# Kernel optimization log

Hardware: AMD Instinct MI355X
Metric: run time of the kernel (lower is better)

## Reference

```python
import jax, jax.numpy as jnp
import numpy as np
import math

DIM = 384
NH = 6
DH = DIM // NH
B = 2
S = 2048
EPS = 1e-6
LN_EPS = 1e-5


def setup_inputs() -> dict:
    key = jax.random.key(0)
    ks = jax.random.split(key, 8)
    q = jax.random.normal(ks[0], (B, S, DIM), dtype=jnp.float32)
    k = jax.random.normal(ks[1], (B, S, DIM), dtype=jnp.float32)
    v = jax.random.normal(ks[2], (B, S, DIM), dtype=jnp.float32)
    # gate linear params (Linear(3*dim, num_heads)); small random weights to exercise the math
    igate_w = jax.random.normal(ks[3], (NH, 3 * DIM), dtype=jnp.float32) * 0.02
    igate_b = jax.random.normal(ks[4], (NH,), dtype=jnp.float32) * 0.1
    fgate_w = jax.random.normal(ks[5], (NH, 3 * DIM), dtype=jnp.float32) * 0.02
    fgate_b = jnp.linspace(3.0, 6.0, NH, dtype=jnp.float32)
    # MultiHeadLayerNorm residual weight (stored as delta, effective scale = 1 + w)
    outnorm_weight = jax.random.normal(ks[6], (DIM,), dtype=jnp.float32) * 0.02
    return {"q": q, "k": k, "v": v, "igate_w": igate_w, "igate_b": igate_b,
            "fgate_w": fgate_w, "fgate_b": fgate_b, "outnorm_weight": outnorm_weight}


def _mlstm_forward(q, k, v, igate_w, igate_b, fgate_w, fgate_b, outnorm_weight):
    Bq, Sq, _ = q.shape
    gate_in = jnp.concatenate([q, k, v], axis=-1)                       # (B,S,3D)
    ig = gate_in @ igate_w.T + igate_b                                   # (B,S,NH)
    fg = gate_in @ fgate_w.T + fgate_b                                   # (B,S,NH)
    # split heads: (B,NH,S,DH)
    qh = q.reshape(Bq, Sq, NH, DH).transpose(0, 2, 1, 3)
    kh = k.reshape(Bq, Sq, NH, DH).transpose(0, 2, 1, 3)
    vh = v.reshape(Bq, Sq, NH, DH).transpose(0, 2, 1, 3)
    ig = ig.transpose(0, 2, 1)                                           # (B,NH,S)
    fg = fg.transpose(0, 2, 1)                                           # (B,NH,S)

    log_fg = jax.nn.log_sigmoid(fg)                                      # (B,NH,S)
    lfc = jnp.concatenate([jnp.zeros((Bq, NH, 1), dtype=q.dtype),
                           jnp.cumsum(log_fg, axis=-1)], axis=-1)        # (B,NH,S+1)
    # log_fg_matrix[i,j] = cumsum[i] - cumsum[j] (sliced [1:,1:]), masked causal
    diff = lfc[:, :, 1:, None] - lfc[:, :, None, 1:]                     # (B,NH,S,S)
    ltr = jnp.tril(jnp.ones((Sq, Sq), dtype=bool))
    log_fg_mat = jnp.where(ltr, diff, -jnp.inf)
    log_D = log_fg_mat + ig[:, :, None, :]                               # + igate^T
    max_log_D = jnp.max(log_D, axis=-1, keepdims=True)                   # rowwise stabilize
    D = jnp.exp(log_D - max_log_D)
    qk = jnp.einsum('bhsd,bhtd->bhst', qh, kh) / math.sqrt(DH)
    C = qk * D
    normalizer = jnp.maximum(jnp.abs(jnp.sum(C, axis=-1, keepdims=True)),
                             jnp.exp(-max_log_D))
    h = jnp.einsum('bhst,bhtd->bhsd', C / (normalizer + EPS), vh)        # (B,NH,S,DH)

    # MultiHeadLayerNorm == group_norm over each head's DH channels, scale=(1+w)
    mean = jnp.mean(h, axis=-1, keepdims=True)
    var = jnp.var(h, axis=-1, keepdims=True)
    normed = (h - mean) / jnp.sqrt(var + LN_EPS)
    scale = (1.0 + outnorm_weight).reshape(NH, DH)[None, :, None, :]
    out = normed * scale
    return out.transpose(0, 2, 1, 3).reshape(Bq, Sq, DIM)


def reference(q, k, v, igate_w, igate_b, fgate_w, fgate_b, outnorm_weight):
    return _mlstm_forward(q, k, v, igate_w, igate_b, fgate_w, fgate_b, outnorm_weight)
```

## Files before the change

### kernel.cpp

```cpp
#include <hip/hip_runtime.h>
#include <math.h>

#define DIM 384
#define NH 6
#define DH 64
#define B_ 2
#define S_ 2048
#define EPS 1e-6f
#define LN_EPS 1e-5f
#define G3 (3*DIM)
#define LOG2E 1.44269504f
#define KSTR 72
#define NT (S_/64)
#define NSPLIT 4
#define NBH (B_*NH)

typedef __attribute__((ext_vector_type(8))) short bf16x8;
typedef __attribute__((ext_vector_type(4))) short bf16x4;
typedef __attribute__((ext_vector_type(4))) float f32x4;
typedef __attribute__((ext_vector_type(8))) unsigned short u16x8;

__device__ __forceinline__ unsigned short f2bf(float f){
    unsigned int u = __float_as_uint(f);
    u += 0x7fff + ((u >> 16) & 1);
    return (unsigned short)(u >> 16);
}
__device__ __forceinline__ float bf2f(unsigned short u){
    return __uint_as_float(((unsigned int)u) << 16);
}
__device__ __forceinline__ float logsig(float x){
    return fminf(x, 0.f) - log1pf(expf(-fabsf(x)));
}

__global__ __launch_bounds__(256) void vt_kernel(
    const float* __restrict__ v, unsigned short* __restrict__ Vt) {
    __shared__ unsigned short lt[64*KSTR];
    int bh = blockIdx.y;
    int b = bh / NH, h = bh % NH;
    int t0 = blockIdx.x * 64;
    int tid = threadIdx.x;
    #pragma unroll
    for (int i = 0; i < 4; i++){
        int idx = tid + 256*i;
        int r = idx >> 4;
        int c4 = (idx & 15) * 4;
        float4 x = *(const float4*)(v + ((size_t)b*S_ + t0 + r)*DIM + h*DH + c4);
        lt[(c4+0)*KSTR + r] = f2bf(x.x);
        lt[(c4+1)*KSTR + r] = f2bf(x.y);
        lt[(c4+2)*KSTR + r] = f2bf(x.z);
        lt[(c4+3)*KSTR + r] = f2bf(x.w);
    }
    __syncthreads();
    #pragma unroll
    for (int i = 0; i < 2; i++){
        int idx = tid + 256*i;
        int d = idx >> 3;
        int t8 = (idx & 7) * 8;
        u16x8 o = *(const u16x8*)&lt[d*KSTR + t8];
        *(u16x8*)(Vt + (size_t)bh*DH*S_ + (size_t)d*S_ + t0 + t8) = o;
    }
}

__global__ __launch_bounds__(256) void gates_kernel(
    const float* __restrict__ q, const float* __restrict__ k, const float* __restrict__ v,
    const float* __restrict__ iw, const float* __restrict__ ib,
    const float* __restrict__ fw, const float* __restrict__ fb,
    float* __restrict__ ig_out, float* __restrict__ lf_out,
    unsigned short* __restrict__ Qb, unsigned short* __restrict__ Kb) {
    int wave = (blockIdx.x * 256 + threadIdx.x) >> 6;
    int lane = threadIdx.x & 63;
    int b = wave / S_, s = wave % S_;
    size_t base = ((size_t)b * S_ + s) * DIM;
    float aI[NH], aF[NH];
    #pragma unroll
    for (int h = 0; h < NH; h++){ aI[h] = 0.f; aF[h] = 0.f; }
    for (int g = lane; g < G3/4; g += 64) {
        int e = g * 4;
        float4 x4;
        if (e < DIM){
            x4 = *(const float4*)(q + base + e);
            ushort4 t; t.x=f2bf(x4.x*0.125f); t.y=f2bf(x4.y*0.125f);
            t.z=f2bf(x4.z*0.125f); t.w=f2bf(x4.w*0.125f);
            *(ushort4*)(Qb + base + e) = t;
        } else if (e < 2*DIM){
            x4 = *(const float4*)(k + base + e - DIM);
            ushort4 t; t.x=f2bf(x4.x); t.y=f2bf(x4.y); t.z=f2bf(x4.z); t.w=f2bf(x4.w);
            *(ushort4*)(Kb + base + e - DIM) = t;
        } else {
            x4 = *(const float4*)(v + base + e - 2*DIM);
        }
        #pragma unroll
        for (int h = 0; h < NH; h++){
            float4 wi = *(const float4*)(iw + h*G3 + e);
            float4 wf = *(const float4*)(fw + h*G3 + e);
            aI[h] = fmaf(x4.x, wi.x, fmaf(x4.y, wi.y, fmaf(x4.z, wi.z, fmaf(x4.w, wi.w, aI[h]))));
            aF[h] = fmaf(x4.x, wf.x, fmaf(x4.y, wf.y, fmaf(x4.z, wf.z, fmaf(x4.w, wf.w, aF[h]))));
        }
    }
    #pragma unroll
    for (int h = 0; h < NH; h++){
        #pragma unroll
        for (int off = 32; off >= 1; off >>= 1){
            aI[h] += __shfl_xor(aI[h], off, 64);
            aF[h] += __shfl_xor(aF[h], off, 64);
        }
    }
    if (lane == 0) {
        #pragma unroll
        for (int h = 0; h < NH; h++){
            ig_out[((size_t)b*NH + h)*S_ + s] = aI[h] + ib[h];
            lf_out[((size_t)b*NH + h)*S_ + s] = logsig(aF[h] + fb[h]);
        }
    }
}

__global__ __launch_bounds__(256) void scan_kernel(
    const float* __restrict__ lf, const float* __restrict__ ig,
    float* __restrict__ cum, float* __restrict__ e2, float* __restrict__ pm,
    float* __restrict__ me, float* __restrict__ baseA){
    int bh = blockIdx.x;
    const float* srcL = lf + (size_t)bh * S_;
    const float* srcI = ig + (size_t)bh * S_;
    float* dstC = cum + (size_t)bh * S_;
    float* dstE = e2 + (size_t)bh * S_;
    float* dstP = pm + (size_t)bh * S_;
    int tid = threadIdx.x;
    float loc[8];
    float run = 0.f;
    #pragma unroll
    for (int j = 0; j < 8; j++){ run += srcL[tid*8 + j]; loc[j] = run; }
    __shared__ float sm[256];
    sm[tid] = run;
    __syncthreads();
    float total = run;
    for (int off = 1; off < 256; off <<= 1){
        float vv = (tid >= off) ? sm[tid - off] : 0.f;
        __syncthreads();
        sm[tid] += vv;
        __syncthreads();
    }
    float excl = sm[tid] - total;
    float c[8];
    #pragma unroll
    for (int j = 0; j < 8; j++){ c[j] = excl + loc[j]; dstC[tid*8 + j] = c[j]; }
    __shared__ float sb[32];
    if ((tid & 7) == 0) sb[tid >> 3] = excl;
    __syncthreads();
    float base_t = sb[tid >> 3];
    float E[8], mloc = -INFINITY;
    #pragma unroll
    for (int j = 0; j < 8; j++){
        E[j] = srcI[tid*8 + j] - c[j] + base_t;
        dstE[tid*8 + j] = exp2f(E[j] * LOG2E);
        mloc = fmaxf(mloc, E[j]);
    }
    __shared__ float smax[256];
    smax[tid] = mloc;
    __syncthreads();
    float carry = -INFINITY;
    int g0 = tid & ~7;
    for (int u = g0; u < tid; u++) carry = fmaxf(carry, smax[u]);
    float runm = carry;
    #pragma unroll
    for (int j = 0; j < 8; j++){
        runm = fmaxf(runm, E[j]);
        dstP[tid*8 + j] = runm;
    }
    if ((tid & 7) == 7) me[bh*NT + (tid >> 3)] = runm;
    if ((tid & 7) == 0) baseA[bh*NT + (tid >> 3)] = base_t;
}

__global__ __launch_bounds__(256) void mlstm_part(
    const unsigned short* __restrict__ Qb, const unsigned short* __restrict__ Kb,
    const unsigned short* __restrict__ Vt,
    const float* __restrict__ cum, const float* __restrict__ e2,
    const float* __restrict__ pm, const float* __restrict__ me,
    const float* __restrict__ baseA,
    unsigned short* __restrict__ pOb, float* __restrict__ pM, float* __restrict__ pL) {
    int lin = blockIdx.x;
    int sp  = lin / NBH;
    int bh  = lin % NBH;
    int st  = (NT - 1) - (sp >> 2);
    int c   = sp & 3;
    int L   = (st + 4) >> 2;
    int tb0 = c * L;
    int tb1 = min((c + 1) * L, st + 1);
    int pblk = lin;
    int tid = threadIdx.x;

    if (tb0 >= tb1){
        if (tid < 64){ pM[pblk*64 + tid] = -INFINITY; pL[pblk*64 + tid] = 0.f; }
        return;
    }

    __shared__ unsigned short kt[2][64*KSTR];
    __shared__ unsigned short vt[2][64*KSTR];

    int b = bh / NH, h = bh % NH;
    int s0 = st * 64;
    int wv   = tid >> 6;
    int lane = tid & 63;
    int lq   = lane & 15;
    int quad = lane >> 4;

    const unsigned short* kbT = Kb + (size_t)b*S_*DIM + h*DH;
    const unsigned short* vtB = Vt + (size_t)bh*DH*S_;
    const float* cmb = cum + (size_t)bh*S_;
    const float* e2b = e2 + (size_t)bh*S_;
    const float* meB = me + bh*NT;
    const float* baseB = baseA + bh*NT;

    int s_glob = s0 + 16*wv + lq;

    bf16x8 qf[2];
    {
        const unsigned short* qr = Qb + ((size_t)b*S_ + s_glob)*DIM + h*DH;
        qf[0] = *(const bf16x8*)(qr + 8*quad);
        qf[1] = *(const bf16x8*)(qr + 32 + 8*quad);
    }

    float cq   = cmb[s_glob];
    float pm_s = pm[(size_t)bh*S_ + s_glob];
    float m_s = -INFINITY, b_s = 0.f;
    f32x4 oacc[4];
    #pragma unroll
    for (int cg = 0; cg < 4; cg++) oacc[cg] = (f32x4){0.f,0.f,0.f,0.f};

    int sr[2], sc[2];
    #pragma unroll
    for (int i = 0; i < 2; i++){
        int idx = tid + 256*i;
        sr[i] = idx >> 3;
        sc[i] = (idx & 7) * 8;
    }

    u16x8 kreg[2], vreg[2];
    {
        const unsigned short* kb = kbT + (size_t)(tb0*64)*DIM;
        const unsigned short* vb = vtB + tb0*64;
        #pragma unroll
        for (int i = 0; i < 2; i++){
            kreg[i] = *(const u16x8*)(kb + (size_t)sr[i]*DIM + sc[i]);
            vreg[i] = *(const u16x8*)(vb + (size_t)sr[i]*S_ + sc[i]);
        }
        #pragma unroll
        for (int i = 0; i < 2; i++){
            *(u16x8*)&kt[0][sr[i]*KSTR + sc[i]] = kreg[i];
            *(u16x8*)&vt[0][sr[i]*KSTR + sc[i]] = vreg[i];
        }
    }
    __syncthreads();

    int bufi = 0;
    for (int t0 = tb0*64; t0 < tb1*64; t0 += 64){
        bool more = (t0 + 64 < tb1*64);
        if (more){
            const unsigned short* kb = kbT + (size_t)(t0 + 64)*DIM;
            const unsigned short* vb = vtB + (t0 + 64);
            #pragma unroll
            for (int i = 0; i < 2; i++){
                kreg[i] = *(const u16x8*)(kb + (size_t)sr[i]*DIM + sc[i]);
                vreg[i] = *(const u16x8*)(vb + (size_t)sr[i]*S_ + sc[i]);
            }
        }

        int tix = t0 >> 6;
        float base_t = baseB[tix];
        float me_t   = meB[tix];
        float4 e2v[4];
        #pragma unroll
        for (int tb = 0; tb < 4; tb++)
            e2v[tb] = *(const float4*)(e2b + t0 + 16*tb + 4*quad);

        const unsigned short* ktc = kt[bufi];
        const unsigned short* vtc = vt[bufi];
        f32x4 st4[4];
        #pragma unroll
        for (int tb = 0; tb < 4; tb++) st4[tb] = (f32x4){0.f,0.f,0.f,0.f};
        #pragma unroll
        for (int ks = 0; ks < 2; ks++){
            #pragma unroll
            for (int tb = 0; tb < 4; tb++){
                bf16x8 af = *(const bf16x8*)&ktc[(16*tb + lq)*KSTR + 32*ks + 8*quad];
                st4[tb] = __builtin_amdgcn_mfma_f32_16x16x32_bf16(af, qf[ks], st4[tb], 0, 0, 0);
            }
        }

        bool diag = (t0 == s0);
        float A = cq - base_t;
        float pmax = A + (diag ? pm_s : me_t);
        float mn = fmaxf(m_s, pmax);
        float sc2 = exp2f((m_s - mn) * LOG2E);
        float ws = exp2f((A - mn) * LOG2E);
        m_s = mn;
        float pv[4][4];
        #pragma unroll
        for (int tb = 0; tb < 4; tb++)
            #pragma unroll
            for (int r = 0; r < 4; r++)
                pv[tb][r] = st4[tb][r] * (ws * e2v[tb][r]);
        if (diag){
            #pragma unroll
            for (int tb = 0; tb < 4; tb++)
                #pragma unroll
                for (int r = 0; r < 4; r++)
                    if (t0 + 16*tb + 4*quad + r > s_glob) pv[tb][r] = 0.f;
        }
        float rs = 0.f;
        bf16x4 pf[4];
        #pragma unroll
        for (int tb = 0; tb < 4; tb++){
            #pragma unroll
            for (int r = 0; r < 4; r++){
                rs += pv[tb][r];
                pf[tb][r] = (short)f2bf(pv[tb][r]);
            }
        }
        rs += __shfl_xor(rs, 16, 64);
        rs += __shfl_xor(rs, 32, 64);
        b_s = b_s * sc2 + rs;

        #pragma unroll
        for (int r = 0; r < 4; r++){
            float sco = __shfl(sc2, 20*quad + r, 64);
            #pragma unroll
            for (int cg = 0; cg < 4; cg++) oacc[cg][r] *= sco;
        }

        #pragma unroll
        for (int tb = 0; tb < 4; tb++){
            #pragma unroll
            for (int cg = 0; cg < 4; cg++){
                bf16x4 vf = *(const bf16x4*)&vtc[(16*cg + lq)*KSTR + 16*tb + 4*quad];
                oacc[cg] = __builtin_amdgcn_mfma_f32_16x16x16bf16_1k(pf[tb], vf, oacc[cg], 0, 0, 0);
            }
        }

        if (more){
            #pragma unroll
            for (int i = 0; i < 2; i++){
                *(u16x8*)&kt[bufi^1][sr[i]*KSTR + sc[i]] = kreg[i];
                *(u16x8*)&vt[bufi^1][sr[i]*KSTR + sc[i]] = vreg[i];
            }
            __syncthreads();
            bufi ^= 1;
        }
    }

    unsigned short* po = pOb + (size_t)pblk * 4096;
    #pragma unroll
    for (int r = 0; r < 4; r++){
        int row = 16*wv + 4*quad + r;
        #pragma unroll
        for (int cg = 0; cg < 4; cg++)
            po[row*64 + 16*cg + lq] = f2bf(oacc[cg][r]);
    }
    if (quad == 0){
        pM[pblk*64 + 16*wv + lq] = m_s;
        pL[pblk*64 + 16*wv + lq] = b_s;
    }
}

__global__ __launch_bounds__(256) void mlstm_combine(
    const unsigned short* __restrict__ pOb, const float* __restrict__ pM,
    const float* __restrict__ pL, const float* __restrict__ w,
    float* __restrict__ out) {
    int st = blockIdx.x;
    int bh = blockIdx.y;
    int b = bh / NH, h = bh % NH;
    int tid = threadIdx.x;
    int cl = (tid & 15) * 4;
    int rb = tid >> 4;

    int pblk[NSPLIT];
    #pragma unroll
    for (int p = 0; p < NSPLIT; p++)
        pblk[p] = (((NT - 1 - st) << 2) + p) * NBH + bh;

    float4 wv4 = *(const float4*)(w + h*DH + cl);

    #pragma unroll
    for (int pass = 0; pass < 4; pass++){
        int row = pass*16 + rb;
        float mp[NSPLIT], lp[NSPLIT];
        float mmax = -INFINITY;
        #pragma unroll
        for (int p = 0; p < NSPLIT; p++){
            mp[p] = pM[pblk[p]*64 + row];
            lp[p] = pL[pblk[p]*64 + row];
            mmax = fmaxf(mmax, mp[p]);
        }
        float l = 0.f;
        float ox = 0.f, oy = 0.f, oz = 0.f, ow = 0.f;
        #pragma unroll
        for (int p = 0; p < NSPLIT; p++){
            if (mp[p] != -INFINITY){
                float wp = exp2f((mp[p] - mmax) * LOG2E);
                l += wp * lp[p];
                ushort4 t4 = *(const ushort4*)(pOb + (size_t)pblk[p]*4096 + row*64 + cl);
                ox += wp*bf2f(t4.x); oy += wp*bf2f(t4.y);
                oz += wp*bf2f(t4.z); ow += wp*bf2f(t4.w);
            }
        }
        float nrm = fmaxf(fabsf(l), exp2f(-mmax * LOG2E));
        float inv = 1.f / (nrm + EPS);
        float x[4] = {ox*inv, oy*inv, oz*inv, ow*inv};
        float s1 = x[0]+x[1]+x[2]+x[3];
        float s2 = x[0]*x[0]+x[1]*x[1]+x[2]*x[2]+x[3]*x[3];
        #pragma unroll
        for (int off = 8; off >= 1; off >>= 1){
            s1 += __shfl_xor(s1, off, 64);
            s2 += __shfl_xor(s2, off, 64);
        }
        float mean = s1 * (1.f/64.f);
        float var  = s2 * (1.f/64.f) - mean*mean;
        float rstd = rsqrtf(var + LN_EPS);
        float4 oo;
        oo.x = (x[0]-mean)*rstd*(1.f + wv4.x);
        oo.y = (x[1]-mean)*rstd*(1.f + wv4.y);
        oo.z = (x[2]-mean)*rstd*(1.f + wv4.z);
        oo.w = (x[3]-mean)*rstd*(1.f + wv4.w);
        *(float4*)(out + ((size_t)b*S_ + st*64 + row)*DIM + h*DH + cl) = oo;
    }
}

extern "C" void kernel_launch(void* const* d_in, const int* in_sizes, int n_in,
                              void* d_out, int out_size, void* d_ws, size_t ws_size,
                              hipStream_t stream) {
    const float* q  = (const float*)d_in[0];
    const float* k  = (const float*)d_in[1];
    const float* v  = (const float*)d_in[2];
    const float* iw = (const float*)d_in[3];
    const float* ib = (const float*)d_in[4];
    const float* fw = (const float*)d_in[5];
    const float* fb = (const float*)d_in[6];
    const float* w  = (const float*)d_in[7];
    float* out = (float*)d_out;

    const int nPart = NBH * NT * NSPLIT;
    const size_t NE = (size_t)B_ * S_ * DIM;
    float* ig   = (float*)d_ws;
    float* lf   = ig   + (size_t)NBH*S_;
    float* cum  = lf   + (size_t)NBH*S_;
    float* e2   = cum  + (size_t)NBH*S_;
    float* pm   = e2   + (size_t)NBH*S_;
    float* me   = pm   + (size_t)NBH*S_;
    float* base = me   + (size_t)NBH*NT;
    float* pM   = base + (size_t)NBH*NT;
    float* pL   = pM   + (size_t)nPart*64;
    unsigned short* pOb = (unsigned short*)(pL + (size_t)nPart*64);
    unsigned short* Qb  = pOb + (size_t)nPart*4096;
    unsigned short* Kb  = Qb + NE;
    unsigned short* Vt  = Kb + NE;

    vt_kernel<<<dim3(NT, NBH), 256, 0, stream>>>(v, Vt);
    gates_kernel<<<B_*S_/4, 256, 0, stream>>>(q, k, v, iw, ib, fw, fb, ig, lf, Qb, Kb);
    scan_kernel<<<NBH, 256, 0, stream>>>(lf, ig, cum, e2, pm, me, base);
    mlstm_part<<<nPart, 256, 0, stream>>>(Qb, Kb, Vt, cum, e2, pm, me, base, pOb, pM, pL);
    mlstm_combine<<<dim3(NT, NBH), 256, 0, stream>>>(pOb, pM, pL, w, out);
}
```

Before: 133.5 us.

## Precompute per-row max to drop online rescaling; fuse V transpose into gates kernel

```diff
diff --git a/kernel.cpp b/kernel.cpp
--- a/kernel.cpp
+++ b/kernel.cpp
@@ -14,6 +14,7 @@
 #define NT (S_/64)
 #define NSPLIT 4
 #define NBH (B_*NH)
+#define NGATE (B_*S_/4)
 
 typedef __attribute__((ext_vector_type(8))) short bf16x8;
 typedef __attribute__((ext_vector_type(4))) short bf16x4;
@@ -30,35 +31,6 @@
 }
 __device__ __forceinline__ float logsig(float x){
     return fminf(x, 0.f) - log1pf(expf(-fabsf(x)));
-}
-
-__global__ __launch_bounds__(256) void vt_kernel(
-    const float* __restrict__ v, unsigned short* __restrict__ Vt) {
-    __shared__ unsigned short lt[64*KSTR];
-    int bh = blockIdx.y;
-    int b = bh / NH, h = bh % NH;
-    int t0 = blockIdx.x * 64;
-    int tid = threadIdx.x;
-    #pragma unroll
-    for (int i = 0; i < 4; i++){
-        int idx = tid + 256*i;
-        int r = idx >> 4;
-        int c4 = (idx & 15) * 4;
-        float4 x = *(const float4*)(v + ((size_t)b*S_ + t0 + r)*DIM + h*DH + c4);
-        lt[(c4+0)*KSTR + r] = f2bf(x.x);
-        lt[(c4+1)*KSTR + r] = f2bf(x.y);
-        lt[(c4+2)*KSTR + r] = f2bf(x.z);
-        lt[(c4+3)*KSTR + r] = f2bf(x.w);
-    }
-    __syncthreads();
-    #pragma unroll
-    for (int i = 0; i < 2; i++){
-        int idx = tid + 256*i;
-        int d = idx >> 3;
-        int t8 = (idx & 7) * 8;
-        u16x8 o = *(const u16x8*)&lt[d*KSTR + t8];
-        *(u16x8*)(Vt + (size_t)bh*DH*S_ + (size_t)d*S_ + t0 + t8) = o;
-    }
 }
 
 __global__ __launch_bounds__(256) void gates_kernel(
@@ -66,9 +38,39 @@
     const float* __restrict__ iw, const float* __restrict__ ib,
     const float* __restrict__ fw, const float* __restrict__ fb,
     float* __restrict__ ig_out, float* __restrict__ lf_out,
-    unsigned short* __restrict__ Qb, unsigned short* __restrict__ Kb) {
-    int wave = (blockIdx.x * 256 + threadIdx.x) >> 6;
-    int lane = threadIdx.x & 63;
+    unsigned short* __restrict__ Qb, unsigned short* __restrict__ Kb,
+    unsigned short* __restrict__ Vt) {
+    __shared__ unsigned short lt[64*KSTR];
+    int tid = threadIdx.x;
+    if (blockIdx.x >= NGATE){
+        int lin = blockIdx.x - NGATE;
+        int bh = lin / NT;
+        int t0 = (lin % NT) * 64;
+        int b = bh / NH, h = bh % NH;
+        #pragma unroll
+        for (int i = 0; i < 4; i++){
+            int idx = tid + 256*i;
+            int r = idx >> 4;
+            int c4 = (idx & 15) * 4;
+            float4 x = *(const float4*)(v + ((size_t)b*S_ + t0 + r)*DIM + h*DH + c4);
+            lt[(c4+0)*KSTR + r] = f2bf(x.x);
+            lt[(c4+1)*KSTR + r] = f2bf(x.y);
+            lt[(c4+2)*KSTR + r] = f2bf(x.z);
+            lt[(c4+3)*KSTR + r] = f2bf(x.w);
+        }
+        __syncthreads();
+        #pragma unroll
+        for (int i = 0; i < 2; i++){
+            int idx = tid + 256*i;
+            int d = idx >> 3;
+            int t8 = (idx & 7) * 8;
+            u16x8 o = *(const u16x8*)&lt[d*KSTR + t8];
+            *(u16x8*)(Vt + (size_t)bh*DH*S_ + (size_t)d*S_ + t0 + t8) = o;
+        }
+        return;
+    }
+    int wave = (blockIdx.x * 256 + tid) >> 6;
+    int lane = tid & 63;
     int b = wave / S_, s = wave % S_;
     size_t base = ((size_t)b * S_ + s) * DIM;
     float aI[NH], aF[NH];
@@ -117,7 +119,7 @@
 __global__ __launch_bounds__(256) void scan_kernel(
     const float* __restrict__ lf, const float* __restrict__ ig,
     float* __restrict__ cum, float* __restrict__ e2, float* __restrict__ pm,
-    float* __restrict__ me, float* __restrict__ baseA){
+    float* __restrict__ gA, float* __restrict__ baseA){
     int bh = blockIdx.x;
     const float* srcL = lf + (size_t)bh * S_;
     const float* srcI = ig + (size_t)bh * S_;
@@ -166,7 +168,7 @@
         runm = fmaxf(runm, E[j]);
         dstP[tid*8 + j] = runm;
     }
-    if ((tid & 7) == 7) me[bh*NT + (tid >> 3)] = runm;
+    if ((tid & 7) == 7) gA[bh*NT + (tid >> 3)] = runm - base_t;
     if ((tid & 7) == 0) baseA[bh*NT + (tid >> 3)] = base_t;
 }
 
@@ -174,7 +176,7 @@
     const unsigned short* __restrict__ Qb, const unsigned short* __restrict__ Kb,
     const unsigned short* __restrict__ Vt,
     const float* __restrict__ cum, const float* __restrict__ e2,
-    const float* __restrict__ pm, const float* __restrict__ me,
+    const float* __restrict__ pm, const float* __restrict__ gA,
     const float* __restrict__ baseA,
     unsigned short* __restrict__ pOb, float* __restrict__ pM, float* __restrict__ pL) {
     int lin = blockIdx.x;
@@ -207,7 +209,7 @@
     const unsigned short* vtB = Vt + (size_t)bh*DH*S_;
     const float* cmb = cum + (size_t)bh*S_;
     const float* e2b = e2 + (size_t)bh*S_;
-    const float* meB = me + bh*NT;
+    const float* gB = gA + bh*NT;
     const float* baseB = baseA + bh*NT;
 
     int s_glob = s0 + 16*wv + lq;
@@ -221,7 +223,14 @@
 
     float cq   = cmb[s_glob];
     float pm_s = pm[(size_t)bh*S_ + s_glob];
-    float m_s = -INFINITY, b_s = 0.f;
+
+    float m = -INFINITY;
+    for (int tix = tb0; tix < tb1; tix++)
+        if (tix != st) m = fmaxf(m, gB[tix]);
+    if (tb1 == st + 1) m = fmaxf(m, pm_s - baseB[st]);
+    float mn = cq + m;
+
+    float b_loc = 0.f;
     f32x4 oacc[4];
     #pragma unroll
     for (int cg = 0; cg < 4; cg++) oacc[cg] = (f32x4){0.f,0.f,0.f,0.f};
@@ -266,7 +275,7 @@
 
         int tix = t0 >> 6;
         float base_t = baseB[tix];
-        float me_t   = meB[tix];
+        float ws = exp2f(-(m + base_t) * LOG2E);
         float4 e2v[4];
         #pragma unroll
         for (int tb = 0; tb < 4; tb++)
@@ -287,12 +296,6 @@
         }
 
         bool diag = (t0 == s0);
-        float A = cq - base_t;
-        float pmax = A + (diag ? pm_s : me_t);
-        float mn = fmaxf(m_s, pmax);
-        float sc2 = exp2f((m_s - mn) * LOG2E);
-        float ws = exp2f((A - mn) * LOG2E);
-        m_s = mn;
         float pv[4][4];
         #pragma unroll
         for (int tb = 0; tb < 4; tb++)
@@ -306,25 +309,14 @@
                 for (int r = 0; r < 4; r++)
                     if (t0 + 16*tb + 4*quad + r > s_glob) pv[tb][r] = 0.f;
         }
-        float rs = 0.f;
         bf16x4 pf[4];
         #pragma unroll
         for (int tb = 0; tb < 4; tb++){
             #pragma unroll
             for (int r = 0; r < 4; r++){
-                rs += pv[tb][r];
+                b_loc += pv[tb][r];
                 pf[tb][r] = (short)f2bf(pv[tb][r]);
             }
-        }
-        rs += __shfl_xor(rs, 16, 64);
-        rs += __shfl_xor(rs, 32, 64);
-        b_s = b_s * sc2 + rs;
-
-        #pragma unroll
-        for (int r = 0; r < 4; r++){
-            float sco = __shfl(sc2, 20*quad + r, 64);
-            #pragma unroll
-            for (int cg = 0; cg < 4; cg++) oacc[cg][r] *= sco;
         }
 
         #pragma unroll
@@ -347,6 +339,8 @@
         }
     }
 
+    b_loc += __shfl_xor(b_loc, 16, 64);
+    b_loc += __shfl_xor(b_loc, 32, 64);
     unsigned short* po = pOb + (size_t)pblk * 4096;
     #pragma unroll
     for (int r = 0; r < 4; r++){
@@ -356,8 +350,8 @@
             po[row*64 + 16*cg + lq] = f2bf(oacc[cg][r]);
     }
     if (quad == 0){
-        pM[pblk*64 + 16*wv + lq] = m_s;
-        pL[pblk*64 + 16*wv + lq] = b_s;
+        pM[pblk*64 + 16*wv + lq] = mn;
+        pL[pblk*64 + 16*wv + lq] = b_loc;
     }
 }
 
@@ -444,8 +438,8 @@
     float* cum  = lf   + (size_t)NBH*S_;
     float* e2   = cum  + (size_t)NBH*S_;
     float* pm   = e2   + (size_t)NBH*S_;
-    float* me   = pm   + (size_t)NBH*S_;
-    float* base = me   + (size_t)NBH*NT;
+    float* gA   = pm   + (size_t)NBH*S_;
+    float* base = gA   + (size_t)NBH*NT;
     float* pM   = base + (size_t)NBH*NT;
     float* pL   = pM   + (size_t)nPart*64;
     unsigned short* pOb = (unsigned short*)(pL + (size_t)nPart*64);
@@ -453,9 +447,9 @@
     unsigned short* Kb  = Qb + NE;
     unsigned short* Vt  = Kb + NE;
 
-    vt_kernel<<<dim3(NT, NBH), 256, 0, stream>>>(v, Vt);
-    gates_kernel<<<B_*S_/4, 256, 0, stream>>>(q, k, v, iw, ib, fw, fb, ig, lf, Qb, Kb);
-    scan_kernel<<<NBH, 256, 0, stream>>>(lf, ig, cum, e2, pm, me, base);
-    mlstm_part<<<nPart, 256, 0, stream>>>(Qb, Kb, Vt, cum, e2, pm, me, base, pOb, pM, pL);
+    gates_kernel<<<NGATE + NBH*NT, 256, 0, stream>>>(q, k, v, iw, ib, fw, fb,
+                                                     ig, lf, Qb, Kb, Vt);
+    scan_kernel<<<NBH, 256, 0, stream>>>(lf, ig, cum, e2, pm, gA, base);
+    mlstm_part<<<nPart, 256, 0, stream>>>(Qb, Kb, Vt, cum, e2, pm, gA, base, pOb, pM, pL);
     mlstm_combine<<<dim3(NT, NBH), 256, 0, stream>>>(pOb, pM, pL, w, out);
 }
```

Result: faster. 128.2 us (median of 2 runs) (-4.0%).
